# Kernel optimization log

Hardware: AMD Instinct MI355X
Metric: run time of the kernel (lower is better)

## Reference

```python
import jax, jax.numpy as jnp
import numpy as np

B, N, M, D, H = 8, 4096, 1024, 1024, 16
HD = D // H  # head_dim = 64
SCALE = HD ** -0.5
EPS = 1e-6


def _ln(x, g, b):
    mu = jnp.mean(x, axis=-1, keepdims=True)
    var = jnp.mean((x - mu) ** 2, axis=-1, keepdims=True)
    return (x - mu) * jax.lax.rsqrt(var + EPS) * g + b


def setup_inputs() -> dict:
    key = jax.random.key(0)
    ks = jax.random.split(key, 10)
    s = 0.02
    return {
        "x": jax.random.normal(ks[0], (B, N, D), jnp.float32),
        "wavelet_tokens": jax.random.normal(ks[1], (B, M, D), jnp.float32),
        "ln_q_g": jnp.ones((D,), jnp.float32),
        "ln_q_b": jnp.zeros((D,), jnp.float32),
        "Wq": jax.random.normal(ks[2], (D, D), jnp.float32) * s,
        "bq": jnp.zeros((D,), jnp.float32),
        "ln_kv_g": jnp.ones((D,), jnp.float32),
        "ln_kv_b": jnp.zeros((D,), jnp.float32),
        "Wkv": jax.random.normal(ks[3], (D, 2 * D), jnp.float32) * s,
        "bkv": jnp.zeros((2 * D,), jnp.float32),
        "Wo": jax.random.normal(ks[4], (D, D), jnp.float32) * s,
        "bo": jnp.zeros((D,), jnp.float32),
        "ln_f_g": jnp.ones((D,), jnp.float32),
        "ln_f_b": jnp.zeros((D,), jnp.float32),
        "W1": jax.random.normal(ks[5], (D, 4 * D), jnp.float32) * s,
        "b1": jnp.zeros((4 * D,), jnp.float32),
        "W2": jax.random.normal(ks[6], (4 * D, D), jnp.float32) * s,
        "b2": jnp.zeros((D,), jnp.float32),
    }


def reference(x, wavelet_tokens, ln_q_g, ln_q_b, Wq, bq, ln_kv_g, ln_kv_b,
              Wkv, bkv, Wo, bo, ln_f_g, ln_f_b, W1, b1, W2, b2):
    residual = x
    q = _ln(x, ln_q_g, ln_q_b) @ Wq + bq            # [B,N,D]
    kv = _ln(wavelet_tokens, ln_kv_g, ln_kv_b) @ Wkv + bkv  # [B,M,2D]
    k, v = kv[..., :D], kv[..., D:]
    q = q.reshape(B, N, H, HD).transpose(0, 2, 1, 3)  # [B,H,N,d]
    k = k.reshape(B, M, H, HD).transpose(0, 2, 1, 3)  # [B,H,M,d]
    v = v.reshape(B, M, H, HD).transpose(0, 2, 1, 3)
    q = jax.nn.softmax(q, axis=2) * SCALE   # softmax over spatial N
    k = jax.nn.softmax(k, axis=-1)          # softmax over head_dim
    context = jnp.einsum('bhmd,bhme->bhde', k, v)   # [B,H,d,d]
    out = jnp.einsum('bhnd,bhde->bhne', q, context)  # [B,H,N,d]
    out = out.transpose(0, 2, 1, 3).reshape(B, N, D)
    out = out @ Wo + bo
    x2 = residual + out
    h = _ln(x2, ln_f_g, ln_f_b) @ W1 + b1
    h = jax.nn.silu(h) @ W2 + b2
    return x2 + h
```

## Files before the change

### kernel.cpp

```cpp
#include <hip/hip_runtime.h>
#include <stdint.h>
#include <stddef.h>

#define BB 8
#define NN 4096
#define MTOK 1024
#define DD 1024
#define HH 16
#define EPSF 1e-6f
static const float SCALE_F = 0.125f;

typedef __attribute__((ext_vector_type(4))) float f32x4;
typedef __attribute__((ext_vector_type(8))) short bf16x8;

__device__ __forceinline__ short f2bf(float f) {
  union { float f; uint32_t u; } x; x.f = f;
  uint32_t r = (x.u + 0x7fffu + ((x.u >> 16) & 1u)) >> 16;
  return (short)(uint16_t)r;
}
__device__ __forceinline__ float bf2f(short s) {
  union { uint32_t u; float f; } x; x.u = ((uint32_t)(uint16_t)s) << 16;
  return x.f;
}

#if defined(__HIP_DEVICE_COMPILE__) && __has_builtin(__builtin_amdgcn_global_load_lds)
#define USE_GLOAD_LDS 1
#else
#define USE_GLOAD_LDS 0
#endif

#define BAR() __builtin_amdgcn_s_barrier()
#define LGKM0() asm volatile("s_waitcnt lgkmcnt(0)" ::: "memory")
#define LGKM8() asm volatile("s_waitcnt lgkmcnt(8)" ::: "memory")
#if USE_GLOAD_LDS
#define VMW6() asm volatile("s_waitcnt vmcnt(6)" ::: "memory")
#else
#define VMW6() asm volatile("s_waitcnt vmcnt(0) lgkmcnt(0)" ::: "memory")
#endif
#define VMW0() asm volatile("s_waitcnt vmcnt(0)" ::: "memory")

__device__ __forceinline__ bf16x8 ldsld(const char* p, int off) {
  return *(const bf16x8*)(p + off);
}
template <int MH>
__device__ __forceinline__ void rdA8(const char* k0, const char* k1, bf16x8 a[4][2]) {
#pragma unroll
  for (int m = 0; m < 4; ++m) {
    a[m][0] = ldsld(k0, MH * 8192 + m * 2048);
    a[m][1] = ldsld(k1, MH * 8192 + m * 2048);
  }
}
template <int NH>
__device__ __forceinline__ void rdB4(const char* k0, const char* k1, bf16x8 b[2][2]) {
#pragma unroll
  for (int n = 0; n < 2; ++n) {
    b[n][0] = ldsld(k0, NH * 16384 + n * 2048);
    b[n][1] = ldsld(k1, NH * 16384 + n * 2048);
  }
}
__device__ __forceinline__ void stgA(char* smc, int base, const short* pg,
                                     int ld, int mh, int k, int w) {
#pragma unroll
  for (int i = 0; i < 2; ++i) {
    const short* src = pg + (long)(mh * 64 + i * 128) * ld + k;
    char* dst = smc + base + i * 16384 + mh * 8192 + w * 1024;
#if USE_GLOAD_LDS
    __builtin_amdgcn_global_load_lds(
        (const __attribute__((address_space(1))) void*)src,
        (__attribute__((address_space(3))) void*)dst, 16, 0, 0);
#else
    *(bf16x8*)(dst + (int)(threadIdx.x & 63) * 16) = *(const bf16x8*)src;
#endif
  }
}
__device__ __forceinline__ void stgB(char* smc, int base, const short* pg,
                                     int ld, int h, int k, int w) {
#pragma unroll
  for (int i = 0; i < 2; ++i) {
    const short* src = pg + (long)(h * 32 + i * 128) * ld + k;
    char* dst = smc + base + h * 16384 + i * 8192 + w * 1024;
#if USE_GLOAD_LDS
    __builtin_amdgcn_global_load_lds(
        (const __attribute__((address_space(1))) void*)src,
        (__attribute__((address_space(3))) void*)dst, 16, 0, 0);
#else
    *(bf16x8*)(dst + (int)(threadIdx.x & 63) * 16) = *(const bf16x8*)src;
#endif
  }
}
template <int MH, int NH>
__device__ __forceinline__ void mq(const bf16x8 a[4][2], const bf16x8 b[2][2],
                                   f32x4 acc[8][4]) {
  __builtin_amdgcn_s_setprio(1);
#pragma unroll
  for (int m = 0; m < 4; ++m)
#pragma unroll
    for (int n = 0; n < 2; ++n) {
      f32x4 c = acc[MH * 4 + m][NH * 2 + n];
      c = __builtin_amdgcn_mfma_f32_16x16x32_bf16(a[m][0], b[n][0], c, 0, 0, 0);
      c = __builtin_amdgcn_mfma_f32_16x16x32_bf16(a[m][1], b[n][1], c, 0, 0, 0);
      acc[MH * 4 + m][NH * 2 + n] = c;
    }
  __builtin_amdgcn_s_setprio(0);
}

template <int EPI>
__global__ __launch_bounds__(512, 2) void gemm256(
    const short* __restrict__ A, const short* __restrict__ BT,
    const float* __restrict__ bias, const void* __restrict__ resid,
    void* __restrict__ outp, int N, int K, int lda, int ldb, int num_n) {
  __shared__ int4 smem4[131072 / 16];
  char* smc = (char*)smem4;
  const int t = threadIdx.x;
  const int w = t >> 6, lane = t & 63;
  const int wr = w >> 2, wc = w & 3;

  const int nwg = gridDim.x, orig = blockIdx.x;
  const int q8 = nwg >> 3, r8 = nwg & 7;
  const int xcd = orig & 7, loc = orig >> 3;
  const int wg = (xcd < r8 ? xcd * (q8 + 1) : r8 * (q8 + 1) + (xcd - r8) * q8) + loc;
  const int bm = wg / num_n, bn = wg % num_n;

  const int T = K >> 6;

  int LA = wr * 16384 + (lane & 15) * 128 + ((lane >> 4) << 4);
  LA ^= ((LA >> 7) & 7) << 4;
  int LB = wc * 4096 + (lane & 15) * 128 + ((lane >> 4) << 4);
  LB ^= ((LB >> 7) & 7) << 4;
  const char* pA0k0 = smc + LA;
  const char* pA0k1 = smc + (LA ^ 64);
  const char* pA1k0 = pA0k0 + 65536;
  const char* pA1k1 = pA0k1 + 65536;
  const char* pB0k0 = smc + 32768 + LB;
  const char* pB0k1 = smc + 32768 + (LB ^ 64);
  const char* pB1k0 = pB0k0 + 65536;
  const char* pB1k1 = pB0k1 + 65536;

  const int colswz = ((t & 7) ^ ((t >> 3) & 7)) * 8;
  const short* pAg = A + (long)(bm * 256 + (t >> 3)) * lda + colswz;
  const short* pBg =
      BT + (long)(bn * 256 + ((t >> 8) * 64 + ((t >> 3) & 31))) * ldb + colswz;

  f32x4 acc[8][4];
#pragma unroll
  for (int i = 0; i < 8; ++i)
#pragma unroll
    for (int j = 0; j < 4; ++j) acc[i][j] = (f32x4){0.f, 0.f, 0.f, 0.f};

  bf16x8 a[4][2], b0[2][2], b1[2][2];

  stgA(smc, 0, pAg, lda, 0, 0, w);
  stgB(smc, 32768, pBg, ldb, 0, 0, w);
  stgB(smc, 32768, pBg, ldb, 1, 0, w);
  stgA(smc, 0, pAg, lda, 1, 0, w);
  stgA(smc, 65536, pAg, lda, 0, 64, w);
  stgB(smc, 98304, pBg, ldb, 0, 64, w);
  stgB(smc, 98304, pBg, ldb, 1, 64, w);
  VMW6();
  BAR();

  for (int t2 = 0; t2 < T; t2 += 2) {
    const int k1 = (t2 + 1) * 64;
    const int k2 = (t2 + 2 < T ? t2 + 2 : 0) * 64;
    const int k3 = (t2 + 3 < T ? t2 + 3 : 0) * 64;
    rdA8<0>(pA0k0, pA0k1, a);
    rdB4<0>(pB0k0, pB0k1, b0);
    stgA(smc, 65536, pAg, lda, 1, k1, w);
    LGKM8();
    BAR(); LGKM0();
    mq<0, 0>(a, b0, acc);
    BAR();
    rdB4<1>(pB0k0, pB0k1, b1);
    stgA(smc, 0, pAg, lda, 0, k2, w);
    BAR(); LGKM0();
    mq<0, 1>(a, b1, acc);
    BAR();
    rdA8<1>(pA0k0, pA0k1, a);
    stgB(smc, 32768, pBg, ldb, 0, k2, w);
    BAR(); LGKM0();
    mq<1, 0>(a, b0, acc);
    BAR();
    stgB(smc, 32768, pBg, ldb, 1, k2, w);
    VMW6();
    BAR();
    mq<1, 1>(a, b1, acc);
    BAR();
    rdA8<0>(pA1k0, pA1k1, a);
    rdB4<0>(pB1k0, pB1k1, b0);
    stgA(smc, 0, pAg, lda, 1, k2, w);
    LGKM8();
    BAR(); LGKM0();
    mq<0, 0>(a, b0, acc);
    BAR();
    rdB4<1>(pB1k0, pB1k1, b1);
    stgA(smc, 65536, pAg, lda, 0, k3, w);
    BAR(); LGKM0();
    mq<0, 1>(a, b1, acc);
    BAR();
    rdA8<1>(pA1k0, pA1k1, a);
    stgB(smc, 98304, pBg, ldb, 0, k3, w);
    BAR(); LGKM0();
    mq<1, 0>(a, b0, acc);
    BAR();
    stgB(smc, 98304, pBg, ldb, 1, k3, w);
    VMW6();
    BAR();
    mq<1, 1>(a, b1, acc);
    BAR();
  }
  VMW0();

  const int r0 = bm * 256 + wr * 128 + ((lane >> 4) << 2);
  const int c0 = bn * 256 + wc * 64 + (lane & 15);
#pragma unroll
  for (int mi = 0; mi < 8; ++mi) {
#pragma unroll
    for (int ni = 0; ni < 4; ++ni) {
      const int col = c0 + ni * 16;
      const float bv = bias ? bias[col] : 0.f;
#pragma unroll
      for (int rr = 0; rr < 4; ++rr) {
        const int row = r0 + mi * 16 + rr;
        const long idx = (long)row * N + col;
        float v = acc[mi][ni][rr] + bv;
        if (EPI == 0) {
          ((float*)outp)[idx] = v;
        } else if (EPI == 1) {
          ((float*)outp)[idx] = v + ((const float*)resid)[idx];
        } else if (EPI == 2) {
          ((short*)outp)[idx] = f2bf(v);
        } else if (EPI == 3) {
          v = v / (1.f + __expf(-v));
          ((short*)outp)[idx] = f2bf(v);
        } else if (EPI == 4) {
          ((short*)outp)[idx] = f2bf(v + ((const float*)resid)[idx]);
        } else {
          ((float*)outp)[idx] = v + bf2f(((const short*)resid)[idx]);
        }
      }
    }
  }
}

__global__ __launch_bounds__(256) void ln_rows(const float* __restrict__ in,
                                               const float* __restrict__ g,
                                               const float* __restrict__ bta,
                                               short* __restrict__ outp) {
  const int row = blockIdx.x;
  const int t = threadIdx.x;
  const float4 v = ((const float4*)(in + (long)row * DD))[t];
  float s = v.x + v.y + v.z + v.w;
  float ss = v.x * v.x + v.y * v.y + v.z * v.z + v.w * v.w;
#pragma unroll
  for (int off = 1; off < 64; off <<= 1) {
    s += __shfl_xor(s, off);
    ss += __shfl_xor(ss, off);
  }
  __shared__ float red[8];
  const int w = t >> 6, lane = t & 63;
  if (lane == 0) { red[w] = s; red[4 + w] = ss; }
  __syncthreads();
  s = red[0] + red[1] + red[2] + red[3];
  ss = red[4] + red[5] + red[6] + red[7];
  const float mu = s * (1.f / DD);
  const float var = ss * (1.f / DD) - mu * mu;
  const float rs = rsqrtf(var + EPSF);
  const float4 gv = ((const float4*)g)[t];
  const float4 bv = ((const float4*)bta)[t];
  short4 o;
  o.x = f2bf((v.x - mu) * rs * gv.x + bv.x);
  o.y = f2bf((v.y - mu) * rs * gv.y + bv.y);
  o.z = f2bf((v.z - mu) * rs * gv.z + bv.z);
  o.w = f2bf((v.w - mu) * rs * gv.w + bv.w);
  ((short4*)(outp + (long)row * DD))[t] = o;
}

__global__ __launch_bounds__(256) void ln_rows_b(const short* __restrict__ in,
                                                 const float* __restrict__ g,
                                                 const float* __restrict__ bta,
                                                 short* __restrict__ outp) {
  const int row = blockIdx.x;
  const int t = threadIdx.x;
  const short4 v4 = ((const short4*)(in + (long)row * DD))[t];
  const float v0 = bf2f(v4.x), v1 = bf2f(v4.y), v2 = bf2f(v4.z), v3 = bf2f(v4.w);
  float s = v0 + v1 + v2 + v3;
  float ss = v0 * v0 + v1 * v1 + v2 * v2 + v3 * v3;
#pragma unroll
  for (int off = 1; off < 64; off <<= 1) {
    s += __shfl_xor(s, off);
    ss += __shfl_xor(ss, off);
  }
  __shared__ float red[8];
  const int w = t >> 6, lane = t & 63;
  if (lane == 0) { red[w] = s; red[4 + w] = ss; }
  __syncthreads();
  s = red[0] + red[1] + red[2] + red[3];
  ss = red[4] + red[5] + red[6] + red[7];
  const float mu = s * (1.f / DD);
  const float var = ss * (1.f / DD) - mu * mu;
  const float rs = rsqrtf(var + EPSF);
  const float4 gv = ((const float4*)g)[t];
  const float4 bv = ((const float4*)bta)[t];
  short4 o;
  o.x = f2bf((v0 - mu) * rs * gv.x + bv.x);
  o.y = f2bf((v1 - mu) * rs * gv.y + bv.y);
  o.z = f2bf((v2 - mu) * rs * gv.z + bv.z);
  o.w = f2bf((v3 - mu) * rs * gv.w + bv.w);
  ((short4*)(outp + (long)row * DD))[t] = o;
}

__global__ __launch_bounds__(256) void tconv(const float* __restrict__ W,
                                             short* __restrict__ WT, int K, int N) {
  __shared__ float tile[64][65];
  const int k0 = blockIdx.x * 64, n0 = blockIdx.y * 64;
  const int t = threadIdx.x;
  const int tr = t >> 6, tc = t & 63;
#pragma unroll
  for (int i = 0; i < 64; i += 4)
    tile[i + tr][tc] = W[(long)(k0 + i + tr) * N + n0 + tc];
  __syncthreads();
#pragma unroll
  for (int i = 0; i < 64; i += 4)
    WT[(long)(n0 + i + tr) * K + k0 + tc] = f2bf(tile[tc][i + tr]);
}

__global__ __launch_bounds__(256) void ctx_kernel(const short* __restrict__ kv,
                                                  float* __restrict__ ctx) {
  const int bh = blockIdx.x;
  const int b = bh >> 4, h = bh & 15;
  const int t = threadIdx.x, g = t >> 6, lane = t & 63;
  __shared__ float ksm[4][64];
  __shared__ float vsm[4][64];
  float acc[16];
#pragma unroll
  for (int j = 0; j < 16; ++j) acc[j] = 0.f;
  const int d = t & 63;
  const int e0 = (t >> 6) * 16;
  const short* base = kv + (long)b * MTOK * 2048 + h * 64;
  for (int m0 = 0; m0 < MTOK; m0 += 4) {
    const long moff = (long)(m0 + g) * 2048;
    float kval = bf2f(base[moff + lane]);
    float vval = bf2f(base[moff + 1024 + lane]);
    float mx = kval;
#pragma unroll
    for (int off = 1; off < 64; off <<= 1) mx = fmaxf(mx, __shfl_xor(mx, off));
    float e = __expf(kval - mx);
    float sm = e;
#pragma unroll
    for (int off = 1; off < 64; off <<= 1) sm += __shfl_xor(sm, off);
    ksm[g][lane] = e / sm;
    vsm[g][lane] = vval;
    __syncthreads();
#pragma unroll
    for (int mm = 0; mm < 4; ++mm) {
      const float kd = ksm[mm][d];
#pragma unroll
      for (int j = 0; j < 16; ++j) acc[j] = fmaf(kd, vsm[mm][e0 + j], acc[j]);
    }
    __syncthreads();
  }
  float* cp = ctx + ((long)bh * 64 + d) * 64 + e0;
#pragma unroll
  for (int j = 0; j < 16; ++j) cp[j] = acc[j];
}

__global__ __launch_bounds__(256) void qstat_part(const short* __restrict__ q,
                                                  float* __restrict__ pmax,
                                                  float* __restrict__ psum) {
  const int c = blockIdx.x * 256 + threadIdx.x;
  const int b = blockIdx.z, ch = blockIdx.y;
  const short* qp = q + ((long)b * NN + ch * 128) * DD + c;
  float mx = -1e30f, sm = 0.f;
  for (int r = 0; r < 128; ++r) {
    const float xv = bf2f(qp[(long)r * DD]);
    const float nm = fmaxf(mx, xv);
    sm = sm * __expf(mx - nm) + __expf(xv - nm);
    mx = nm;
  }
  const long idx = ((long)b * DD + c) * 32 + ch;
  pmax[idx] = mx;
  psum[idx] = sm;
}

__global__ __launch_bounds__(256) void qstat_comb(const float* __restrict__ pmax,
                                                  const float* __restrict__ psum,
                                                  float* __restrict__ cmax,
                                                  float* __restrict__ crs) {
  const int i = blockIdx.x * 256 + threadIdx.x;
  const float* pm = pmax + (long)i * 32;
  const float* ps = psum + (long)i * 32;
  float mx = -1e30f;
#pragma unroll
  for (int ch = 0; ch < 32; ++ch) mx = fmaxf(mx, pm[ch]);
  float sm = 0.f;
#pragma unroll
  for (int ch = 0; ch < 32; ++ch) sm += ps[ch] * __expf(pm[ch] - mx);
  cmax[i] = mx;
  crs[i] = SCALE_F / sm;
}

__global__ __launch_bounds__(256) void attn_apply(const short* __restrict__ q,
                                                  const float* __restrict__ ctx,
                                                  const float* __restrict__ cmax,
                                                  const float* __restrict__ crs,
                                                  short* __restrict__ outa) {
  const int b = blockIdx.z, h = blockIdx.y, n0 = blockIdx.x * 128;
  const int t = threadIdx.x, g = t >> 6, lane = t & 63;
  __shared__ float ctx_l[4096];
  __shared__ float cm[64], cs[64];
  __shared__ float qsm[4][64];
  const float* cp = ctx + (long)(b * HH + h) * 4096;
  for (int i = t; i < 4096; i += 256) ctx_l[i] = cp[i];
  if (t < 64) {
    cm[t] = cmax[(long)b * DD + h * 64 + t];
    cs[t] = crs[(long)b * DD + h * 64 + t];
  }
  __syncthreads();
  for (int i = 0; i < 32; ++i) {
    const int n = n0 + i * 4 + g;
    const long off = ((long)b * NN + n) * DD + h * 64;
    const float qv = bf2f(q[off + lane]);
    const float qs = __expf(qv - cm[lane]) * cs[lane];
    qsm[g][lane] = qs;
    float o = 0.f;
#pragma unroll
    for (int dd = 0; dd < 64; ++dd) o = fmaf(qsm[g][dd], ctx_l[dd * 64 + lane], o);
    outa[off + lane] = f2bf(o);
  }
}

extern "C" void kernel_launch(void* const* d_in, const int* in_sizes, int n_in,
                              void* d_out, int out_size, void* d_ws, size_t ws_size,
                              hipStream_t stream) {
  (void)in_sizes; (void)n_in; (void)out_size;
  const float* x      = (const float*)d_in[0];
  const float* wav    = (const float*)d_in[1];
  const float* ln_q_g = (const float*)d_in[2];
  const float* ln_q_b = (const float*)d_in[3];
  const float* Wq     = (const float*)d_in[4];
  const float* bq     = (const float*)d_in[5];
  const float* ln_kv_g= (const float*)d_in[6];
  const float* ln_kv_b= (const float*)d_in[7];
  const float* Wkv    = (const float*)d_in[8];
  const float* bkv    = (const float*)d_in[9];
  const float* Wo     = (const float*)d_in[10];
  const float* bo     = (const float*)d_in[11];
  const float* ln_f_g = (const float*)d_in[12];
  const float* ln_f_b = (const float*)d_in[13];
  const float* W1     = (const float*)d_in[14];
  const float* b1     = (const float*)d_in[15];
  const float* W2     = (const float*)d_in[16];
  const float* b2     = (const float*)d_in[17];
  float* outp = (float*)d_out;
  char* ws = (char*)d_ws;

  const long MR = (long)BB * NN;
  const long MKV = (long)BB * MTOK;

  size_t off = 0;
  auto bump = [&](size_t bytes) {
    size_t o = off;
    off += (bytes + 255) & ~(size_t)255;
    return o;
  };
  short* WqT  = (short*)(ws + bump((size_t)DD * DD * 2));
  short* WkvT = (short*)(ws + bump((size_t)2048 * DD * 2));
  short* WoT  = (short*)(ws + bump((size_t)DD * DD * 2));
  short* W1T  = (short*)(ws + bump((size_t)4096 * DD * 2));
  short* W2T  = (short*)(ws + bump((size_t)DD * 4096 * 2));
  short* qbuf = (short*)(ws + bump((size_t)MR * DD * 2));
  short* lnbuf= (short*)(ws + bump((size_t)MR * DD * 2));
  float* ctx  = (float*)(ws + bump((size_t)BB * HH * 64 * 64 * 4));
  float* pmax = (float*)(ws + bump((size_t)BB * DD * 32 * 4));
  float* psum = (float*)(ws + bump((size_t)BB * DD * 32 * 4));
  float* cmax = (float*)(ws + bump((size_t)BB * DD * 4));
  float* crs  = (float*)(ws + bump((size_t)BB * DD * 4));
  const size_t dyn0 = off;
  short* wvln  = (short*)(ws + dyn0);
  short* kvbuf = (short*)(ws + dyn0 + (size_t)MKV * DD * 2);
  short* oattn = (short*)(ws + dyn0);
  short* hbuf  = (short*)(ws + dyn0);

  size_t avail = ws_size > dyn0 ? ws_size - dyn0 : 0;
  int CS = 4096;
  while (CS > 256 && (size_t)MR * CS * 2 > avail) CS >>= 1;

  const int nm = (int)(MR / 256);
  const int nmkv = (int)(MKV / 256);

  tconv<<<dim3(DD / 64, DD / 64), 256, 0, stream>>>(Wq, WqT, DD, DD);
  tconv<<<dim3(DD / 64, 2048 / 64), 256, 0, stream>>>(Wkv, WkvT, DD, 2048);
  tconv<<<dim3(DD / 64, DD / 64), 256, 0, stream>>>(Wo, WoT, DD, DD);
  tconv<<<dim3(DD / 64, 4096 / 64), 256, 0, stream>>>(W1, W1T, DD, 4096);
  tconv<<<dim3(4096 / 64, DD / 64), 256, 0, stream>>>(W2, W2T, 4096, DD);

  ln_rows<<<dim3((unsigned)MR), 256, 0, stream>>>(x, ln_q_g, ln_q_b, lnbuf);
  ln_rows<<<dim3((unsigned)MKV), 256, 0, stream>>>(wav, ln_kv_g, ln_kv_b, wvln);

  gemm256<2><<<dim3((unsigned)(nm * (DD / 256))), 512, 0, stream>>>(
      lnbuf, WqT, bq, nullptr, qbuf, DD, DD, DD, DD, DD / 256);
  gemm256<2><<<dim3((unsigned)(nmkv * (2048 / 256))), 512, 0, stream>>>(
      wvln, WkvT, bkv, nullptr, kvbuf, 2048, DD, DD, DD, 2048 / 256);
  ctx_kernel<<<dim3(BB * HH), 256, 0, stream>>>(kvbuf, ctx);
  qstat_part<<<dim3(DD / 256, 32, BB), 256, 0, stream>>>(qbuf, pmax, psum);
  qstat_comb<<<dim3(BB * DD / 256), 256, 0, stream>>>(pmax, psum, cmax, crs);
  attn_apply<<<dim3(NN / 128, HH, BB), 256, 0, stream>>>(qbuf, ctx, cmax, crs, oattn);
  gemm256<4><<<dim3((unsigned)(nm * (DD / 256))), 512, 0, stream>>>(
      oattn, WoT, bo, x, qbuf, DD, DD, DD, DD, DD / 256);
  short* x2b = qbuf;
  ln_rows_b<<<dim3((unsigned)MR), 256, 0, stream>>>(x2b, ln_f_g, ln_f_b, lnbuf);
  for (int c0 = 0; c0 < 4096; c0 += CS) {
    gemm256<3><<<dim3((unsigned)(nm * (CS / 256))), 512, 0, stream>>>(
        lnbuf, W1T + (long)c0 * DD, b1 + c0, nullptr, hbuf, CS, DD, DD, DD, CS / 256);
    if (c0 == 0) {
      gemm256<5><<<dim3((unsigned)(nm * (DD / 256))), 512, 0, stream>>>(
          hbuf, W2T + c0, b2, x2b, outp, DD, CS, CS, 4096, DD / 256);
    } else {
      gemm256<1><<<dim3((unsigned)(nm * (DD / 256))), 512, 0, stream>>>(
          hbuf, W2T + c0, nullptr, outp, outp, DD, CS, CS, 4096, DD / 256);
    }
  }
}
```

Before: 1.261 ms.

## Software-pipeline LDS fragment reads with MFMA via double-buffered A registers

Restructures the GEMM main loop so each step issues the LDS reads for the next MFMA sub-tile before running the current one. A second A-fragment register set makes this possible and halves the barriers per sub-step. The aim is to hide LDS read latency behind matrix-core work and cut synchronisation stalls. In exchange it needs more VGPRs, which may lower occupancy. The reordering of shared-memory reuse against the barriers also carries correctness risk.

```diff
diff --git a/kernel.cpp b/kernel.cpp
--- a/kernel.cpp
+++ b/kernel.cpp
@@ -31,7 +31,6 @@
 
 #define BAR() __builtin_amdgcn_s_barrier()
 #define LGKM0() asm volatile("s_waitcnt lgkmcnt(0)" ::: "memory")
-#define LGKM8() asm volatile("s_waitcnt lgkmcnt(8)" ::: "memory")
 #if USE_GLOAD_LDS
 #define VMW6() asm volatile("s_waitcnt vmcnt(6)" ::: "memory")
 #else
@@ -147,7 +146,7 @@
 #pragma unroll
     for (int j = 0; j < 4; ++j) acc[i][j] = (f32x4){0.f, 0.f, 0.f, 0.f};
 
-  bf16x8 a[4][2], b0[2][2], b1[2][2];
+  bf16x8 a0[4][2], a1[4][2], b0[2][2], b1[2][2];
 
   stgA(smc, 0, pAg, lda, 0, 0, w);
   stgB(smc, 32768, pBg, ldb, 0, 0, w);
@@ -158,56 +157,57 @@
   stgB(smc, 98304, pBg, ldb, 1, 64, w);
   VMW6();
   BAR();
+  rdA8<0>(pA0k0, pA0k1, a0);
+  rdB4<0>(pB0k0, pB0k1, b0);
 
   for (int t2 = 0; t2 < T; t2 += 2) {
     const int k1 = (t2 + 1) * 64;
     const int k2 = (t2 + 2 < T ? t2 + 2 : 0) * 64;
     const int k3 = (t2 + 3 < T ? t2 + 3 : 0) * 64;
-    rdA8<0>(pA0k0, pA0k1, a);
+    LGKM0();
+    rdB4<1>(pB0k0, pB0k1, b1);
+    stgA(smc, 65536, pAg, lda, 1, k1, w);
+    mq<0, 0>(a0, b0, acc);
+    BAR();
+    LGKM0();
+    rdA8<1>(pA0k0, pA0k1, a1);
+    stgA(smc, 0, pAg, lda, 0, k2, w);
+    mq<0, 1>(a0, b1, acc);
+    BAR();
+    LGKM0();
+    stgB(smc, 32768, pBg, ldb, 0, k2, w);
+    mq<1, 0>(a1, b0, acc);
+    BAR();
+    LGKM0();
+    VMW6();
+    rdA8<0>(pA1k0, pA1k1, a0);
+    rdB4<0>(pB1k0, pB1k1, b0);
+    stgB(smc, 32768, pBg, ldb, 1, k2, w);
+    mq<1, 1>(a1, b1, acc);
+    BAR();
+    LGKM0();
+    rdB4<1>(pB1k0, pB1k1, b1);
+    stgA(smc, 0, pAg, lda, 1, k2, w);
+    mq<0, 0>(a0, b0, acc);
+    BAR();
+    LGKM0();
+    rdA8<1>(pA1k0, pA1k1, a1);
+    stgA(smc, 65536, pAg, lda, 0, k3, w);
+    mq<0, 1>(a0, b1, acc);
+    BAR();
+    LGKM0();
+    stgB(smc, 98304, pBg, ldb, 0, k3, w);
+    mq<1, 0>(a1, b0, acc);
+    BAR();
+    LGKM0();
+    VMW6();
+    rdA8<0>(pA0k0, pA0k1, a0);
     rdB4<0>(pB0k0, pB0k1, b0);
-    stgA(smc, 65536, pAg, lda, 1, k1, w);
-    LGKM8();
-    BAR(); LGKM0();
-    mq<0, 0>(a, b0, acc);
-    BAR();
-    rdB4<1>(pB0k0, pB0k1, b1);
-    stgA(smc, 0, pAg, lda, 0, k2, w);
-    BAR(); LGKM0();
-    mq<0, 1>(a, b1, acc);
-    BAR();
-    rdA8<1>(pA0k0, pA0k1, a);
-    stgB(smc, 32768, pBg, ldb, 0, k2, w);
-    BAR(); LGKM0();
-    mq<1, 0>(a, b0, acc);
-    BAR();
-    stgB(smc, 32768, pBg, ldb, 1, k2, w);
-    VMW6();
-    BAR();
-    mq<1, 1>(a, b1, acc);
-    BAR();
-    rdA8<0>(pA1k0, pA1k1, a);
-    rdB4<0>(pB1k0, pB1k1, b0);
-    stgA(smc, 0, pAg, lda, 1, k2, w);
-    LGKM8();
-    BAR(); LGKM0();
-    mq<0, 0>(a, b0, acc);
-    BAR();
-    rdB4<1>(pB1k0, pB1k1, b1);
-    stgA(smc, 65536, pAg, lda, 0, k3, w);
-    BAR(); LGKM0();
-    mq<0, 1>(a, b1, acc);
-    BAR();
-    rdA8<1>(pA1k0, pA1k1, a);
-    stgB(smc, 98304, pBg, ldb, 0, k3, w);
-    BAR(); LGKM0();
-    mq<1, 0>(a, b0, acc);
-    BAR();
     stgB(smc, 98304, pBg, ldb, 1, k3, w);
-    VMW6();
-    BAR();
-    mq<1, 1>(a, b1, acc);
-    BAR();
-  }
+    mq<1, 1>(a1, b1, acc);
+    BAR();
+  }
+  LGKM0();
   VMW0();
 
   const int r0 = bm * 256 + wr * 128 + ((lane >> 4) << 2);
```

After: 1.340 ms. +6.3%, slower.
